# Kernel tuning notes

Hardware: AMD Instinct MI355X
Metric: run time of the kernel (lower is better)

Reference implementation:

```python
import jax, jax.numpy as jnp
import numpy as np

N, T, IN_DIM = 5000, 100, 32
FEAT, HID, OUT, HEADS = 64, 64, 8, 4
E = 160000
F_IN = FEAT + OUT  # GATCell input = concat(embedding, theta)


def setup_inputs() -> dict:
    key = jax.random.key(0)
    ks = jax.random.split(key, 16)
    s = 0.05
    d = {}
    d["x"] = jax.random.normal(ks[0], (N, T, IN_DIM), jnp.float32)
    d["edge_index"] = jax.random.randint(ks[1], (2, E), 0, N, dtype=jnp.int32)
    # LSTM params (PyTorch gate order: i, f, g, o)
    d["W_ih"] = jax.random.normal(ks[2], (IN_DIM, 4 * FEAT), jnp.float32) * s
    d["W_hh"] = jax.random.normal(ks[3], (FEAT, 4 * FEAT), jnp.float32) * s
    d["b_ih"] = jax.random.normal(ks[4], (4 * FEAT,), jnp.float32) * s
    d["b_hh"] = jax.random.normal(ks[5], (4 * FEAT,), jnp.float32) * s
    # TransformerConv params (lin_q/k/v with bias, lin_skip with bias; concat=False)
    d["Wq"] = jax.random.normal(ks[6], (F_IN, HEADS * HID), jnp.float32) * s
    d["bq"] = jax.random.normal(ks[7], (HEADS * HID,), jnp.float32) * s
    d["Wk"] = jax.random.normal(ks[8], (F_IN, HEADS * HID), jnp.float32) * s
    d["bk"] = jax.random.normal(ks[9], (HEADS * HID,), jnp.float32) * s
    d["Wv"] = jax.random.normal(ks[10], (F_IN, HEADS * HID), jnp.float32) * s
    d["bv"] = jax.random.normal(ks[11], (HEADS * HID,), jnp.float32) * s
    d["Wskip"] = jax.random.normal(ks[12], (F_IN, HID), jnp.float32) * s
    d["bskip"] = jax.random.normal(ks[13], (HID,), jnp.float32) * s
    # GATCell mlp (bias=False)
    d["Wmlp"] = jax.random.normal(ks[14], (HID, OUT), jnp.float32) * s
    return d


def _lstm(x, W_ih, W_hh, b_ih, b_hh):
    # x: [N, T, IN_DIM] -> embedding [T, N, FEAT]
    xs = jnp.transpose(x, (1, 0, 2))

    def step(carry, xt):
        h, c = carry
        gates = xt @ W_ih + h @ W_hh + (b_ih + b_hh)
        i, f, g, o = jnp.split(gates, 4, axis=-1)
        c = jax.nn.sigmoid(f) * c + jax.nn.sigmoid(i) * jnp.tanh(g)
        h = jax.nn.sigmoid(o) * jnp.tanh(c)
        return (h, c), h

    h0 = jnp.zeros((x.shape[0], FEAT), x.dtype)
    _, hs = jax.lax.scan(step, (h0, h0), xs)
    return hs


def _transformer_conv(h, edge_index, Wq, bq, Wk, bk, Wv, bv, Wskip, bskip):
    # h: [N, F_IN]; edge_index: [2, E] (row 0 = source j, row 1 = target i)
    n = h.shape[0]
    src, dst = edge_index[0], edge_index[1]
    q = (h @ Wq + bq).reshape(n, HEADS, HID)
    k = (h @ Wk + bk).reshape(n, HEADS, HID)
    v = (h @ Wv + bv).reshape(n, HEADS, HID)
    # per-edge attention logits [E, HEADS]
    alpha = jnp.einsum('ehd,ehd->eh', q[dst], k[src]) / jnp.sqrt(jnp.float32(HID))
    # segment softmax over incoming edges of each target node
    m = jax.ops.segment_max(alpha, dst, num_segments=n)
    m = jnp.where(jnp.isfinite(m), m, 0.0)
    ex = jnp.exp(alpha - m[dst])
    denom = jax.ops.segment_sum(ex, dst, num_segments=n)
    w = ex / jnp.maximum(denom[dst], 1e-16)
    agg = jax.ops.segment_sum(w[:, :, None] * v[src], dst, num_segments=n)  # [N,H,D]
    out = agg.mean(axis=1)  # concat=False -> average heads
    return out + h @ Wskip + bskip  # root skip connection


def reference(x, edge_index, W_ih, W_hh, b_ih, b_hh, Wq, bq, Wk, bk, Wv, bv,
              Wskip, bskip, Wmlp):
    emb = _lstm(x, W_ih, W_hh, b_ih, b_hh)  # [T, N, FEAT]
    n = x.shape[0]

    def gat_step(theta, emb_t):
        h_in = jnp.concatenate([emb_t, theta], axis=-1)  # [N, F_IN]
        hid = _transformer_conv(h_in, edge_index, Wq, bq, Wk, bk, Wv, bv,
                                Wskip, bskip)
        theta_new = jnp.tanh(hid) @ Wmlp
        return theta_new, theta_new

    theta0 = jnp.zeros((n, OUT), x.dtype)
    _, thetas = jax.lax.scan(gat_step, theta0, emb)  # [T, N, OUT]
    theta = jnp.transpose(thetas, (1, 0, 2))  # [N, T, OUT]

    alpha_beta = theta[:, :, :-3]
    a_b = jax.nn.sigmoid(theta[:, :, -3:-1])
    a = a_b[:, :, 0:1] * a_b[:, :, 1:]
    b = a_b[:, :, 0:1] - a
    c = jax.nn.softplus(theta[:, :, -1:])
    return jnp.concatenate([alpha_beta, a, b, c], axis=-1)
```

## Files before the change

### kernel.cpp

```cpp
#include <hip/hip_runtime.h>
#include <math.h>

#define NN 5000
#define TT 100
#define IND 32
#define FEATD 64
#define HIDD 64
#define OUTD 8
#define NHEADS 4
#define EE 160000
#define FIN 72
#define NHC 256

typedef unsigned short ushortx4 __attribute__((ext_vector_type(4)));
typedef float floatx2 __attribute__((ext_vector_type(2)));

__device__ __forceinline__ float fsig(float x){ return 1.f/(1.f+__expf(-x)); }
__device__ __forceinline__ float ftanh(float x){ return 1.f - 2.f/(__expf(2.f*x)+1.f); }
__device__ __forceinline__ float fsoftplus(float x){ return (x>20.f)? x : log1pf(__expf(x)); }

__global__ __launch_bounds__(256) void count_edges(const int* __restrict__ dst,
                                                   int* __restrict__ cnt){
    int e = blockIdx.x*256 + threadIdx.x;
    if (e < EE) atomicAdd(&cnt[dst[e]], 1);
}

#define SCAN_N 5120
__global__ __launch_bounds__(1024) void scan_csr(const int* __restrict__ cnt,
                                                 int* __restrict__ row_ptr,
                                                 int* __restrict__ cursor){
    __shared__ int sa[SCAN_N];
    __shared__ int sb[SCAN_N];
    int tid = threadIdx.x;
    for (int i=tid;i<SCAN_N;i+=1024) sa[i] = (i<NN)?cnt[i]:0;
    __syncthreads();
    int *s=sa, *d=sb;
    for (int off=1; off<SCAN_N; off<<=1){
        for (int i=tid;i<SCAN_N;i+=1024){
            int v = s[i];
            if (i>=off) v += s[i-off];
            d[i] = v;
        }
        __syncthreads();
        int* t=s; s=d; d=t;
    }
    for (int i=tid;i<=NN;i+=1024){
        int excl = (i==0)?0:s[i-1];
        row_ptr[i] = excl;
        if (i<NN) cursor[i] = excl;
    }
}

__global__ __launch_bounds__(256) void fill_edges(const int* __restrict__ src,
                                                  const int* __restrict__ dst,
                                                  int* __restrict__ cursor,
                                                  int* __restrict__ col){
    int e = blockIdx.x*256 + threadIdx.x;
    if (e < EE){
        int dn = dst[e];
        int pos = atomicAdd(&cursor[dn], 1);
        col[pos] = src[e];
    }
}

__global__ __launch_bounds__(256) void lstm_qkv_step(
    const float* __restrict__ x,
    const float* __restrict__ W_ih, const float* __restrict__ W_hh,
    const float* __restrict__ b_ih, const float* __restrict__ b_hh,
    const float* __restrict__ Wq, const float* __restrict__ bq,
    const float* __restrict__ Wk, const float* __restrict__ bk,
    const float* __restrict__ Wv, const float* __restrict__ bv,
    const float* __restrict__ Wsk, const float* __restrict__ bsk,
    float* __restrict__ h, float* __restrict__ c,
    const float* __restrict__ theta,
    float* __restrict__ q, float* __restrict__ sk,
    unsigned char* __restrict__ kv, int t)
{
    __shared__ float xh[8][96];
    __shared__ float hin[8][72];
    int n0 = blockIdx.x * 8;
    int tid = threadIdx.x;
    for (int i=tid; i<8*96; i+=256){
        int node = i/96, kk = i%96;
        int n = n0 + node;
        xh[node][kk] = (kk<32) ? x[(n*TT + t)*IND + kk] : h[n*64 + (kk-32)];
    }
    if (tid < 64){
        int node = tid>>3, j = tid&7;
        hin[node][64+j] = theta[(n0+node)*8 + j];
    }
    __syncthreads();

    int d  = tid & 63;
    int wv = tid >> 6;
    float acc[2][4];
    #pragma unroll
    for (int p=0;p<2;p++){
        #pragma unroll
        for (int g=0;g<4;g++) acc[p][g]=0.f;
    }
    #pragma unroll 8
    for (int kk=0; kk<32; kk++){
        const float* Wr = W_ih + kk*256;
        float w0=Wr[d], w1=Wr[d+64], w2=Wr[d+128], w3=Wr[d+192];
        float x0 = xh[wv][kk], x1 = xh[wv+4][kk];
        acc[0][0]=fmaf(x0,w0,acc[0][0]); acc[0][1]=fmaf(x0,w1,acc[0][1]);
        acc[0][2]=fmaf(x0,w2,acc[0][2]); acc[0][3]=fmaf(x0,w3,acc[0][3]);
        acc[1][0]=fmaf(x1,w0,acc[1][0]); acc[1][1]=fmaf(x1,w1,acc[1][1]);
        acc[1][2]=fmaf(x1,w2,acc[1][2]); acc[1][3]=fmaf(x1,w3,acc[1][3]);
    }
    #pragma unroll 8
    for (int kk=0; kk<64; kk++){
        const float* Wr = W_hh + kk*256;
        float w0=Wr[d], w1=Wr[d+64], w2=Wr[d+128], w3=Wr[d+192];
        float x0 = xh[wv][32+kk], x1 = xh[wv+4][32+kk];
        acc[0][0]=fmaf(x0,w0,acc[0][0]); acc[0][1]=fmaf(x0,w1,acc[0][1]);
        acc[0][2]=fmaf(x0,w2,acc[0][2]); acc[0][3]=fmaf(x0,w3,acc[0][3]);
        acc[1][0]=fmaf(x1,w0,acc[1][0]); acc[1][1]=fmaf(x1,w1,acc[1][1]);
        acc[1][2]=fmaf(x1,w2,acc[1][2]); acc[1][3]=fmaf(x1,w3,acc[1][3]);
    }
    float bi0 = b_ih[d]     + b_hh[d];
    float bi1 = b_ih[d+64]  + b_hh[d+64];
    float bi2 = b_ih[d+128] + b_hh[d+128];
    float bi3 = b_ih[d+192] + b_hh[d+192];
    #pragma unroll
    for (int p=0;p<2;p++){
        int node = wv + p*4;
        int n = n0 + node;
        float gi = fsig (acc[p][0] + bi0);
        float gf = fsig (acc[p][1] + bi1);
        float gg = ftanh(acc[p][2] + bi2);
        float go = fsig (acc[p][3] + bi3);
        float cold = c[n*64 + d];
        float cnew = gf*cold + gi*gg;
        float hnew = go*ftanh(cnew);
        c[n*64 + d] = cnew;
        h[n*64 + d] = hnew;
        hin[node][d] = hnew;
    }
    __syncthreads();

    if (tid < 208){
        int c4 = tid*4;
        const float* W; const float* b; int ncol; int cc; int kind;
        if (c4 < 256)      { W=Wq;  b=bq;  ncol=256; cc=c4;     kind=0; }
        else if (c4 < 512) { W=Wk;  b=bk;  ncol=256; cc=c4-256; kind=1; }
        else if (c4 < 768) { W=Wv;  b=bv;  ncol=256; cc=c4-512; kind=2; }
        else               { W=Wsk; b=bsk; ncol=64;  cc=c4-768; kind=3; }
        float acc2[8][4];
        #pragma unroll
        for (int nn=0;nn<8;nn++){
            #pragma unroll
            for (int j=0;j<4;j++) acc2[nn][j]=0.f;
        }
        #pragma unroll 4
        for (int kk=0; kk<FIN; kk++){
            float4 w = *reinterpret_cast<const float4*>(W + kk*ncol + cc);
            #pragma unroll
            for (int nn=0;nn<8;nn++){
                float xv = hin[nn][kk];
                acc2[nn][0]=fmaf(xv,w.x,acc2[nn][0]);
                acc2[nn][1]=fmaf(xv,w.y,acc2[nn][1]);
                acc2[nn][2]=fmaf(xv,w.z,acc2[nn][2]);
                acc2[nn][3]=fmaf(xv,w.w,acc2[nn][3]);
            }
        }
        float4 bb = *reinterpret_cast<const float4*>(b + cc);
        #pragma unroll
        for (int nn=0;nn<8;nn++){
            int n = n0 + nn;
            float o0=acc2[nn][0]+bb.x, o1=acc2[nn][1]+bb.y;
            float o2=acc2[nn][2]+bb.z, o3=acc2[nn][3]+bb.w;
            if (kind == 0){
                float4 o = {o0,o1,o2,o3};
                *reinterpret_cast<float4*>(q + n*NHC + cc) = o;
            } else if (kind == 3){
                float4 o = {o0,o1,o2,o3};
                *reinterpret_cast<float4*>(sk + n*64 + cc) = o;
            } else {
                int pk = __builtin_amdgcn_cvt_pk_fp8_f32(o0, o1, 0,  false);
                pk     = __builtin_amdgcn_cvt_pk_fp8_f32(o2, o3, pk, true);
                int off = n*512 + cc*2 + ((kind==2)?4:0);
                *reinterpret_cast<unsigned int*>(kv + off) = (unsigned int)pk;
            }
        }
    }
}

#define LOADKV(e) (*reinterpret_cast<const uint2*>(kv + (size_t)col[(e)]*512 + lane*8))
__global__ __launch_bounds__(256) void attn_step(const float* __restrict__ q,
                                                 const unsigned char* __restrict__ kv,
                                                 const float* __restrict__ sk,
                                                 const int* __restrict__ row_ptr,
                                                 const int* __restrict__ col,
                                                 const float* __restrict__ Wmlp,
                                                 float* __restrict__ theta,
                                                 float* __restrict__ out,
                                                 int t){
    __shared__ float mrg[2][5][64];
    int wvid = threadIdx.x >> 6;
    int lane = threadIdx.x & 63;
    int ln   = wvid >> 1;
    int half = wvid & 1;
    int n = blockIdx.x*2 + ln;
    int e0 = row_ptr[n], e1 = row_ptr[n+1];
    float4 qv = *reinterpret_cast<const float4*>(q + n*NHC + lane*4);
    qv.x *= 0.125f; qv.y *= 0.125f; qv.z *= 0.125f; qv.w *= 0.125f;

    float denA=0.f, denB=0.f;
    float aA0=0.f, aA1=0.f, aA2=0.f, aA3=0.f;
    float aB0=0.f, aB1=0.f, aB2=0.f, aB3=0.f;

    const uint2 zv = {0u,0u};
    uint2 bA0=zv, bA1=zv, bB0=zv, bB1=zv;
    int base = e0 + half;
    if (base     < e1) bA0 = LOADKV(base);
    if (base + 2 < e1) bB0 = LOADKV(base+2);
    if (base + 4 < e1) bA1 = LOADKV(base+4);
    if (base + 6 < e1) bB1 = LOADKV(base+6);
    for (int e = base; e < e1; e += 4){
        uint2 uA = bA0; bA0 = bA1; bA1 = zv;
        uint2 uB = bB0; bB0 = bB1; bB1 = zv;
        if (e + 8  < e1) bA1 = LOADKV(e+8);
        if (e + 10 < e1) bB1 = LOADKV(e+10);

        floatx2 kA0 = __builtin_amdgcn_cvt_pk_f32_fp8(uA.x, false);
        floatx2 kA1 = __builtin_amdgcn_cvt_pk_f32_fp8(uA.x, true);
        floatx2 kB0 = __builtin_amdgcn_cvt_pk_f32_fp8(uB.x, false);
        floatx2 kB1 = __builtin_amdgcn_cvt_pk_f32_fp8(uB.x, true);
        float pA = qv.x*kA0[0] + qv.y*kA0[1] + qv.z*kA1[0] + qv.w*kA1[1];
        float pB = qv.x*kB0[0] + qv.y*kB0[1] + qv.z*kB1[0] + qv.w*kB1[1];
        pA += __shfl_xor(pA,1); pB += __shfl_xor(pB,1);
        pA += __shfl_xor(pA,2); pB += __shfl_xor(pB,2);
        pA += __shfl_xor(pA,4); pB += __shfl_xor(pB,4);
        pA += __shfl_xor(pA,8); pB += __shfl_xor(pB,8);

        float eA = __expf(pA);
        float eB = __expf((e + 2 < e1) ? pB : -INFINITY);
        floatx2 vA0 = __builtin_amdgcn_cvt_pk_f32_fp8(uA.y, false);
        floatx2 vA1 = __builtin_amdgcn_cvt_pk_f32_fp8(uA.y, true);
        floatx2 vB0 = __builtin_amdgcn_cvt_pk_f32_fp8(uB.y, false);
        floatx2 vB1 = __builtin_amdgcn_cvt_pk_f32_fp8(uB.y, true);
        denA += eA;
        aA0 = fmaf(eA, vA0[0], aA0);
        aA1 = fmaf(eA, vA0[1], aA1);
        aA2 = fmaf(eA, vA1[0], aA2);
        aA3 = fmaf(eA, vA1[1], aA3);
        denB += eB;
        aB0 = fmaf(eB, vB0[0], aB0);
        aB1 = fmaf(eB, vB0[1], aB1);
        aB2 = fmaf(eB, vB1[0], aB2);
        aB3 = fmaf(eB, vB1[1], aB3);
    }
    float denom = denA + denB;
    float ax = aA0 + aB0;
    float ay = aA1 + aB1;
    float az = aA2 + aB2;
    float aw = aA3 + aB3;

    if (half == 1){
        mrg[ln][0][lane]=denom;
        mrg[ln][1][lane]=ax; mrg[ln][2][lane]=ay;
        mrg[ln][3][lane]=az; mrg[ln][4][lane]=aw;
    }
    __syncthreads();
    if (half == 1) return;

    denom += mrg[ln][0][lane];
    ax += mrg[ln][1][lane];
    ay += mrg[ln][2][lane];
    az += mrg[ln][3][lane];
    aw += mrg[ln][4][lane];

    float inv = 1.f / fmaxf(denom, 1e-16f);
    ax *= inv; ay *= inv; az *= inv; aw *= inv;
    ax += __shfl_xor(ax,16); ax += __shfl_xor(ax,32);
    ay += __shfl_xor(ay,16); ay += __shfl_xor(ay,32);
    az += __shfl_xor(az,16); az += __shfl_xor(az,32);
    aw += __shfl_xor(aw,16); aw += __shfl_xor(aw,32);
    int d0 = (lane & 15) * 4;
    float4 skv = *reinterpret_cast<const float4*>(sk + n*64 + d0);
    float t0 = ftanh(0.25f*ax + skv.x);
    float t1 = ftanh(0.25f*ay + skv.y);
    float t2 = ftanh(0.25f*az + skv.z);
    float t3 = ftanh(0.25f*aw + skv.w);
    float p8[8];
    #pragma unroll
    for (int j=0;j<8;j++){
        p8[j] = fmaf(t0, Wmlp[(d0+0)*8+j],
                fmaf(t1, Wmlp[(d0+1)*8+j],
                fmaf(t2, Wmlp[(d0+2)*8+j],
                     t3* Wmlp[(d0+3)*8+j])));
    }
    #pragma unroll
    for (int j=0;j<8;j++){
        p8[j] += __shfl_xor(p8[j],1);
        p8[j] += __shfl_xor(p8[j],2);
        p8[j] += __shfl_xor(p8[j],4);
        p8[j] += __shfl_xor(p8[j],8);
    }
    if (lane == 0){
        float4 t0v = {p8[0],p8[1],p8[2],p8[3]};
        float4 t1v = {p8[4],p8[5],p8[6],p8[7]};
        *reinterpret_cast<float4*>(theta + n*8)     = t0v;
        *reinterpret_cast<float4*>(theta + n*8 + 4) = t1v;
        float ab0 = fsig(p8[5]);
        float ab1 = fsig(p8[6]);
        float a  = ab0*ab1;
        float bb = ab0 - a;
        float cc = fsoftplus(p8[7]);
        float4 o0 = {p8[0],p8[1],p8[2],p8[3]};
        float4 o1 = {p8[4],a,bb,cc};
        float* op = out + ((size_t)n*TT + t)*8;
        *reinterpret_cast<float4*>(op)     = o0;
        *reinterpret_cast<float4*>(op + 4) = o1;
    }
}

extern "C" void kernel_launch(void* const* d_in, const int* in_sizes, int n_in,
                              void* d_out, int out_size, void* d_ws, size_t ws_size,
                              hipStream_t stream) {
    const float* x     = (const float*)d_in[0];
    const int*   ei    = (const int*)  d_in[1];
    const float* W_ih  = (const float*)d_in[2];
    const float* W_hh  = (const float*)d_in[3];
    const float* b_ih  = (const float*)d_in[4];
    const float* b_hh  = (const float*)d_in[5];
    const float* Wq    = (const float*)d_in[6];
    const float* bq    = (const float*)d_in[7];
    const float* Wk    = (const float*)d_in[8];
    const float* bk    = (const float*)d_in[9];
    const float* Wv    = (const float*)d_in[10];
    const float* bv    = (const float*)d_in[11];
    const float* Wsk   = (const float*)d_in[12];
    const float* bsk   = (const float*)d_in[13];
    const float* Wmlp  = (const float*)d_in[14];
    float* out = (float*)d_out;

    float* f = (float*)d_ws;
    float* h     = f;
    float* c     = h + NN*64;
    float* theta = c + NN*64;
    float* q     = theta + NN*8;
    float* skb   = q + NN*NHC;
    unsigned char* kvb = (unsigned char*)(skb + NN*64);
    int* ip      = (int*)(kvb + (size_t)NN*512);
    int* row_ptr = ip;
    int* cnt     = row_ptr + (NN+1);
    int* cursor  = cnt + NN;
    int* colv    = cursor + NN;

    const int* src = ei;
    const int* dst = ei + EE;

    hipMemsetAsync(h, 0, (size_t)NN*(64+64+8)*sizeof(float), stream);
    hipMemsetAsync(cnt, 0, (size_t)NN*sizeof(int), stream);

    count_edges<<<(EE+255)/256, 256, 0, stream>>>(dst, cnt);
    scan_csr<<<1, 1024, 0, stream>>>(cnt, row_ptr, cursor);
    fill_edges<<<(EE+255)/256, 256, 0, stream>>>(src, dst, cursor, colv);

    for (int t=0; t<TT; t++){
        lstm_qkv_step<<<NN/8, 256, 0, stream>>>(x, W_ih, W_hh, b_ih, b_hh,
                                                Wq,bq, Wk,bk, Wv,bv, Wsk,bsk,
                                                h, c, theta, q, skb, kvb, t);
        attn_step<<<NN/2, 256, 0, stream>>>(q, kvb, skb, row_ptr, colv, Wmlp,
                                            theta, out, t);
    }
}
```

Baseline: 5.113 ms.

## Overlap LSTM step t with attention step t-1 in one fused launch

```diff
diff --git a/kernel.cpp b/kernel.cpp
--- a/kernel.cpp
+++ b/kernel.cpp
@@ -11,8 +11,9 @@
 #define EE 160000
 #define FIN 72
 #define NHC 256
-
-typedef unsigned short ushortx4 __attribute__((ext_vector_type(4)));
+#define ATTN_B 2500
+#define LSTM_B 625
+
 typedef float floatx2 __attribute__((ext_vector_type(2)));
 
 __device__ __forceinline__ float fsig(float x){ return 1.f/(1.f+__expf(-x)); }
@@ -63,80 +64,219 @@
     }
 }
 
-__global__ __launch_bounds__(256) void lstm_qkv_step(
+#define LOADKV(e) (*reinterpret_cast<const uint2*>(kv + (size_t)col[(e)]*512 + lane*8))
+__global__ __launch_bounds__(256) void lstm_attn_step(
     const float* __restrict__ x,
     const float* __restrict__ W_ih, const float* __restrict__ W_hh,
     const float* __restrict__ b_ih, const float* __restrict__ b_hh,
+    float* __restrict__ h, float* __restrict__ c,
+    const float* __restrict__ q,
+    const unsigned char* __restrict__ kv,
+    const float* __restrict__ sk,
+    const int* __restrict__ row_ptr,
+    const int* __restrict__ col,
+    const float* __restrict__ Wmlp,
+    float* __restrict__ theta,
+    float* __restrict__ out,
+    int t)
+{
+    __shared__ float mrg[2][5][64];
+    __shared__ float xh[8][96];
+    int tid = threadIdx.x;
+
+    if (blockIdx.x < ATTN_B){
+        if (t == 0) return;
+        int wvid = tid >> 6;
+        int lane = tid & 63;
+        int ln   = wvid >> 1;
+        int half = wvid & 1;
+        int n = blockIdx.x*2 + ln;
+        int e0 = row_ptr[n], e1 = row_ptr[n+1];
+        float4 qv = *reinterpret_cast<const float4*>(q + n*NHC + lane*4);
+        qv.x *= 0.125f; qv.y *= 0.125f; qv.z *= 0.125f; qv.w *= 0.125f;
+
+        float denA=0.f, denB=0.f;
+        float aA0=0.f, aA1=0.f, aA2=0.f, aA3=0.f;
+        float aB0=0.f, aB1=0.f, aB2=0.f, aB3=0.f;
+
+        const uint2 zv = {0u,0u};
+        uint2 bA0=zv, bA1=zv, bB0=zv, bB1=zv;
+        int base = e0 + half;
+        if (base     < e1) bA0 = LOADKV(base);
+        if (base + 2 < e1) bB0 = LOADKV(base+2);
+        if (base + 4 < e1) bA1 = LOADKV(base+4);
+        if (base + 6 < e1) bB1 = LOADKV(base+6);
+        for (int e = base; e < e1; e += 4){
+            uint2 uA = bA0; bA0 = bA1; bA1 = zv;
+            uint2 uB = bB0; bB0 = bB1; bB1 = zv;
+            if (e + 8  < e1) bA1 = LOADKV(e+8);
+            if (e + 10 < e1) bB1 = LOADKV(e+10);
+
+            floatx2 kA0 = __builtin_amdgcn_cvt_pk_f32_fp8(uA.x, false);
+            floatx2 kA1 = __builtin_amdgcn_cvt_pk_f32_fp8(uA.x, true);
+            floatx2 kB0 = __builtin_amdgcn_cvt_pk_f32_fp8(uB.x, false);
+            floatx2 kB1 = __builtin_amdgcn_cvt_pk_f32_fp8(uB.x, true);
+            float pA = qv.x*kA0[0] + qv.y*kA0[1] + qv.z*kA1[0] + qv.w*kA1[1];
+            float pB = qv.x*kB0[0] + qv.y*kB0[1] + qv.z*kB1[0] + qv.w*kB1[1];
+            pA += __shfl_xor(pA,1); pB += __shfl_xor(pB,1);
+            pA += __shfl_xor(pA,2); pB += __shfl_xor(pB,2);
+            pA += __shfl_xor(pA,4); pB += __shfl_xor(pB,4);
+            pA += __shfl_xor(pA,8); pB += __shfl_xor(pB,8);
+
+            float eA = __expf(pA);
+            float eB = __expf((e + 2 < e1) ? pB : -INFINITY);
+            floatx2 vA0 = __builtin_amdgcn_cvt_pk_f32_fp8(uA.y, false);
+            floatx2 vA1 = __builtin_amdgcn_cvt_pk_f32_fp8(uA.y, true);
+            floatx2 vB0 = __builtin_amdgcn_cvt_pk_f32_fp8(uB.y, false);
+            floatx2 vB1 = __builtin_amdgcn_cvt_pk_f32_fp8(uB.y, true);
+            denA += eA;
+            aA0 = fmaf(eA, vA0[0], aA0);
+            aA1 = fmaf(eA, vA0[1], aA1);
+            aA2 = fmaf(eA, vA1[0], aA2);
+            aA3 = fmaf(eA, vA1[1], aA3);
+            denB += eB;
+            aB0 = fmaf(eB, vB0[0], aB0);
+            aB1 = fmaf(eB, vB0[1], aB1);
+            aB2 = fmaf(eB, vB1[0], aB2);
+            aB3 = fmaf(eB, vB1[1], aB3);
+        }
+        float denom = denA + denB;
+        float ax = aA0 + aB0;
+        float ay = aA1 + aB1;
+        float az = aA2 + aB2;
+        float aw = aA3 + aB3;
+
+        if (half == 1){
+            mrg[ln][0][lane]=denom;
+            mrg[ln][1][lane]=ax; mrg[ln][2][lane]=ay;
+            mrg[ln][3][lane]=az; mrg[ln][4][lane]=aw;
+        }
+        __syncthreads();
+        if (half == 1) return;
+
+        denom += mrg[ln][0][lane];
+        ax += mrg[ln][1][lane];
+        ay += mrg[ln][2][lane];
+        az += mrg[ln][3][lane];
+        aw += mrg[ln][4][lane];
+
+        float inv = 1.f / fmaxf(denom, 1e-16f);
+        ax *= inv; ay *= inv; az *= inv; aw *= inv;
+        ax += __shfl_xor(ax,16); ax += __shfl_xor(ax,32);
+        ay += __shfl_xor(ay,16); ay += __shfl_xor(ay,32);
+        az += __shfl_xor(az,16); az += __shfl_xor(az,32);
+        aw += __shfl_xor(aw,16); aw += __shfl_xor(aw,32);
+        int d0 = (lane & 15) * 4;
+        float4 skv = *reinterpret_cast<const float4*>(sk + n*64 + d0);
+        float t0 = ftanh(0.25f*ax + skv.x);
+        float t1 = ftanh(0.25f*ay + skv.y);
+        float t2 = ftanh(0.25f*az + skv.z);
+        float t3 = ftanh(0.25f*aw + skv.w);
+        float p8[8];
+        #pragma unroll
+        for (int j=0;j<8;j++){
+            p8[j] = fmaf(t0, Wmlp[(d0+0)*8+j],
+                    fmaf(t1, Wmlp[(d0+1)*8+j],
+                    fmaf(t2, Wmlp[(d0+2)*8+j],
+                         t3* Wmlp[(d0+3)*8+j])));
+        }
+        #pragma unroll
+        for (int j=0;j<8;j++){
+            p8[j] += __shfl_xor(p8[j],1);
+            p8[j] += __shfl_xor(p8[j],2);
+            p8[j] += __shfl_xor(p8[j],4);
+            p8[j] += __shfl_xor(p8[j],8);
+        }
+        if (lane == 0){
+            float4 t0v = {p8[0],p8[1],p8[2],p8[3]};
+            float4 t1v = {p8[4],p8[5],p8[6],p8[7]};
+            *reinterpret_cast<float4*>(theta + n*8)     = t0v;
+            *reinterpret_cast<float4*>(theta + n*8 + 4) = t1v;
+            float ab0 = fsig(p8[5]);
+            float ab1 = fsig(p8[6]);
+            float a  = ab0*ab1;
+            float bb = ab0 - a;
+            float cc = fsoftplus(p8[7]);
+            float4 o0 = {p8[0],p8[1],p8[2],p8[3]};
+            float4 o1 = {p8[4],a,bb,cc};
+            float* op = out + ((size_t)n*TT + (t-1))*8;
+            *reinterpret_cast<float4*>(op)     = o0;
+            *reinterpret_cast<float4*>(op + 4) = o1;
+        }
+    } else {
+        if (t >= TT) return;
+        int n0 = (blockIdx.x - ATTN_B) * 8;
+        for (int i=tid; i<8*96; i+=256){
+            int node = i/96, kk = i%96;
+            int n = n0 + node;
+            xh[node][kk] = (kk<32) ? x[(n*TT + t)*IND + kk] : h[n*64 + (kk-32)];
+        }
+        __syncthreads();
+
+        int d  = tid & 63;
+        int wv = tid >> 6;
+        float acc[2][4];
+        #pragma unroll
+        for (int p=0;p<2;p++){
+            #pragma unroll
+            for (int g=0;g<4;g++) acc[p][g]=0.f;
+        }
+        #pragma unroll 8
+        for (int kk=0; kk<32; kk++){
+            const float* Wr = W_ih + kk*256;
+            float w0=Wr[d], w1=Wr[d+64], w2=Wr[d+128], w3=Wr[d+192];
+            float x0 = xh[wv][kk], x1 = xh[wv+4][kk];
+            acc[0][0]=fmaf(x0,w0,acc[0][0]); acc[0][1]=fmaf(x0,w1,acc[0][1]);
+            acc[0][2]=fmaf(x0,w2,acc[0][2]); acc[0][3]=fmaf(x0,w3,acc[0][3]);
+            acc[1][0]=fmaf(x1,w0,acc[1][0]); acc[1][1]=fmaf(x1,w1,acc[1][1]);
+            acc[1][2]=fmaf(x1,w2,acc[1][2]); acc[1][3]=fmaf(x1,w3,acc[1][3]);
+        }
+        #pragma unroll 8
+        for (int kk=0; kk<64; kk++){
+            const float* Wr = W_hh + kk*256;
+            float w0=Wr[d], w1=Wr[d+64], w2=Wr[d+128], w3=Wr[d+192];
+            float x0 = xh[wv][32+kk], x1 = xh[wv+4][32+kk];
+            acc[0][0]=fmaf(x0,w0,acc[0][0]); acc[0][1]=fmaf(x0,w1,acc[0][1]);
+            acc[0][2]=fmaf(x0,w2,acc[0][2]); acc[0][3]=fmaf(x0,w3,acc[0][3]);
+            acc[1][0]=fmaf(x1,w0,acc[1][0]); acc[1][1]=fmaf(x1,w1,acc[1][1]);
+            acc[1][2]=fmaf(x1,w2,acc[1][2]); acc[1][3]=fmaf(x1,w3,acc[1][3]);
+        }
+        float bi0 = b_ih[d]     + b_hh[d];
+        float bi1 = b_ih[d+64]  + b_hh[d+64];
+        float bi2 = b_ih[d+128] + b_hh[d+128];
+        float bi3 = b_ih[d+192] + b_hh[d+192];
+        #pragma unroll
+        for (int p=0;p<2;p++){
+            int n = n0 + wv + p*4;
+            float gi = fsig (acc[p][0] + bi0);
+            float gf = fsig (acc[p][1] + bi1);
+            float gg = ftanh(acc[p][2] + bi2);
+            float go = fsig (acc[p][3] + bi3);
+            float cold = c[n*64 + d];
+            float cnew = gf*cold + gi*gg;
+            float hnew = go*ftanh(cnew);
+            c[n*64 + d] = cnew;
+            h[n*64 + d] = hnew;
+        }
+    }
+}
+
+__global__ __launch_bounds__(256) void qkv_step(
+    const float* __restrict__ h, const float* __restrict__ theta,
     const float* __restrict__ Wq, const float* __restrict__ bq,
     const float* __restrict__ Wk, const float* __restrict__ bk,
     const float* __restrict__ Wv, const float* __restrict__ bv,
     const float* __restrict__ Wsk, const float* __restrict__ bsk,
-    float* __restrict__ h, float* __restrict__ c,
-    const float* __restrict__ theta,
     float* __restrict__ q, float* __restrict__ sk,
-    unsigned char* __restrict__ kv, int t)
+    unsigned char* __restrict__ kv)
 {
-    __shared__ float xh[8][96];
     __shared__ float hin[8][72];
     int n0 = blockIdx.x * 8;
     int tid = threadIdx.x;
-    for (int i=tid; i<8*96; i+=256){
-        int node = i/96, kk = i%96;
+    for (int i=tid; i<8*72; i+=256){
+        int node = i/72, kk = i%72;
         int n = n0 + node;
-        xh[node][kk] = (kk<32) ? x[(n*TT + t)*IND + kk] : h[n*64 + (kk-32)];
-    }
-    if (tid < 64){
-        int node = tid>>3, j = tid&7;
-        hin[node][64+j] = theta[(n0+node)*8 + j];
-    }
-    __syncthreads();
-
-    int d  = tid & 63;
-    int wv = tid >> 6;
-    float acc[2][4];
-    #pragma unroll
-    for (int p=0;p<2;p++){
-        #pragma unroll
-        for (int g=0;g<4;g++) acc[p][g]=0.f;
-    }
-    #pragma unroll 8
-    for (int kk=0; kk<32; kk++){
-        const float* Wr = W_ih + kk*256;
-        float w0=Wr[d], w1=Wr[d+64], w2=Wr[d+128], w3=Wr[d+192];
-        float x0 = xh[wv][kk], x1 = xh[wv+4][kk];
-        acc[0][0]=fmaf(x0,w0,acc[0][0]); acc[0][1]=fmaf(x0,w1,acc[0][1]);
-        acc[0][2]=fmaf(x0,w2,acc[0][2]); acc[0][3]=fmaf(x0,w3,acc[0][3]);
-        acc[1][0]=fmaf(x1,w0,acc[1][0]); acc[1][1]=fmaf(x1,w1,acc[1][1]);
-        acc[1][2]=fmaf(x1,w2,acc[1][2]); acc[1][3]=fmaf(x1,w3,acc[1][3]);
-    }
-    #pragma unroll 8
-    for (int kk=0; kk<64; kk++){
-        const float* Wr = W_hh + kk*256;
-        float w0=Wr[d], w1=Wr[d+64], w2=Wr[d+128], w3=Wr[d+192];
-        float x0 = xh[wv][32+kk], x1 = xh[wv+4][32+kk];
-        acc[0][0]=fmaf(x0,w0,acc[0][0]); acc[0][1]=fmaf(x0,w1,acc[0][1]);
-        acc[0][2]=fmaf(x0,w2,acc[0][2]); acc[0][3]=fmaf(x0,w3,acc[0][3]);
-        acc[1][0]=fmaf(x1,w0,acc[1][0]); acc[1][1]=fmaf(x1,w1,acc[1][1]);
-        acc[1][2]=fmaf(x1,w2,acc[1][2]); acc[1][3]=fmaf(x1,w3,acc[1][3]);
-    }
-    float bi0 = b_ih[d]     + b_hh[d];
-    float bi1 = b_ih[d+64]  + b_hh[d+64];
-    float bi2 = b_ih[d+128] + b_hh[d+128];
-    float bi3 = b_ih[d+192] + b_hh[d+192];
-    #pragma unroll
-    for (int p=0;p<2;p++){
-        int node = wv + p*4;
-        int n = n0 + node;
-        float gi = fsig (acc[p][0] + bi0);
-        float gf = fsig (acc[p][1] + bi1);
-        float gg = ftanh(acc[p][2] + bi2);
-        float go = fsig (acc[p][3] + bi3);
-        float cold = c[n*64 + d];
-        float cnew = gf*cold + gi*gg;
-        float hnew = go*ftanh(cnew);
-        c[n*64 + d] = cnew;
-        h[n*64 + d] = hnew;
-        hin[node][d] = hnew;
+        hin[node][kk] = (kk<64) ? h[n*64+kk] : theta[n*8 + (kk-64)];
     }
     __syncthreads();
 
@@ -184,136 +324,6 @@
                 *reinterpret_cast<unsigned int*>(kv + off) = (unsigned int)pk;
             }
         }
-    }
-}
-
-#define LOADKV(e) (*reinterpret_cast<const uint2*>(kv + (size_t)col[(e)]*512 + lane*8))
-__global__ __launch_bounds__(256) void attn_step(const float* __restrict__ q,
-                                                 const unsigned char* __restrict__ kv,
-                                                 const float* __restrict__ sk,
-                                                 const int* __restrict__ row_ptr,
-                                                 const int* __restrict__ col,
-                                                 const float* __restrict__ Wmlp,
-                                                 float* __restrict__ theta,
-                                                 float* __restrict__ out,
-                                                 int t){
-    __shared__ float mrg[2][5][64];
-    int wvid = threadIdx.x >> 6;
-    int lane = threadIdx.x & 63;
-    int ln   = wvid >> 1;
-    int half = wvid & 1;
-    int n = blockIdx.x*2 + ln;
-    int e0 = row_ptr[n], e1 = row_ptr[n+1];
-    float4 qv = *reinterpret_cast<const float4*>(q + n*NHC + lane*4);
-    qv.x *= 0.125f; qv.y *= 0.125f; qv.z *= 0.125f; qv.w *= 0.125f;
-
-    float denA=0.f, denB=0.f;
-    float aA0=0.f, aA1=0.f, aA2=0.f, aA3=0.f;
-    float aB0=0.f, aB1=0.f, aB2=0.f, aB3=0.f;
-
-    const uint2 zv = {0u,0u};
-    uint2 bA0=zv, bA1=zv, bB0=zv, bB1=zv;
-    int base = e0 + half;
-    if (base     < e1) bA0 = LOADKV(base);
-    if (base + 2 < e1) bB0 = LOADKV(base+2);
-    if (base + 4 < e1) bA1 = LOADKV(base+4);
-    if (base + 6 < e1) bB1 = LOADKV(base+6);
-    for (int e = base; e < e1; e += 4){
-        uint2 uA = bA0; bA0 = bA1; bA1 = zv;
-        uint2 uB = bB0; bB0 = bB1; bB1 = zv;
-        if (e + 8  < e1) bA1 = LOADKV(e+8);
-        if (e + 10 < e1) bB1 = LOADKV(e+10);
-
-        floatx2 kA0 = __builtin_amdgcn_cvt_pk_f32_fp8(uA.x, false);
-        floatx2 kA1 = __builtin_amdgcn_cvt_pk_f32_fp8(uA.x, true);
-        floatx2 kB0 = __builtin_amdgcn_cvt_pk_f32_fp8(uB.x, false);
-        floatx2 kB1 = __builtin_amdgcn_cvt_pk_f32_fp8(uB.x, true);
-        float pA = qv.x*kA0[0] + qv.y*kA0[1] + qv.z*kA1[0] + qv.w*kA1[1];
-        float pB = qv.x*kB0[0] + qv.y*kB0[1] + qv.z*kB1[0] + qv.w*kB1[1];
-        pA += __shfl_xor(pA,1); pB += __shfl_xor(pB,1);
-        pA += __shfl_xor(pA,2); pB += __shfl_xor(pB,2);
-        pA += __shfl_xor(pA,4); pB += __shfl_xor(pB,4);
-        pA += __shfl_xor(pA,8); pB += __shfl_xor(pB,8);
-
-        float eA = __expf(pA);
-        float eB = __expf((e + 2 < e1) ? pB : -INFINITY);
-        floatx2 vA0 = __builtin_amdgcn_cvt_pk_f32_fp8(uA.y, false);
-        floatx2 vA1 = __builtin_amdgcn_cvt_pk_f32_fp8(uA.y, true);
-        floatx2 vB0 = __builtin_amdgcn_cvt_pk_f32_fp8(uB.y, false);
-        floatx2 vB1 = __builtin_amdgcn_cvt_pk_f32_fp8(uB.y, true);
-        denA += eA;
-        aA0 = fmaf(eA, vA0[0], aA0);
-        aA1 = fmaf(eA, vA0[1], aA1);
-        aA2 = fmaf(eA, vA1[0], aA2);
-        aA3 = fmaf(eA, vA1[1], aA3);
-        denB += eB;
-        aB0 = fmaf(eB, vB0[0], aB0);
-        aB1 = fmaf(eB, vB0[1], aB1);
-        aB2 = fmaf(eB, vB1[0], aB2);
-        aB3 = fmaf(eB, vB1[1], aB3);
-    }
-    float denom = denA + denB;
-    float ax = aA0 + aB0;
-    float ay = aA1 + aB1;
-    float az = aA2 + aB2;
-    float aw = aA3 + aB3;
-
-    if (half == 1){
-        mrg[ln][0][lane]=denom;
-        mrg[ln][1][lane]=ax; mrg[ln][2][lane]=ay;
-        mrg[ln][3][lane]=az; mrg[ln][4][lane]=aw;
-    }
-    __syncthreads();
-    if (half == 1) return;
-
-    denom += mrg[ln][0][lane];
-    ax += mrg[ln][1][lane];
-    ay += mrg[ln][2][lane];
-    az += mrg[ln][3][lane];
-    aw += mrg[ln][4][lane];
-
-    float inv = 1.f / fmaxf(denom, 1e-16f);
-    ax *= inv; ay *= inv; az *= inv; aw *= inv;
-    ax += __shfl_xor(ax,16); ax += __shfl_xor(ax,32);
-    ay += __shfl_xor(ay,16); ay += __shfl_xor(ay,32);
-    az += __shfl_xor(az,16); az += __shfl_xor(az,32);
-    aw += __shfl_xor(aw,16); aw += __shfl_xor(aw,32);
-    int d0 = (lane & 15) * 4;
-    float4 skv = *reinterpret_cast<const float4*>(sk + n*64 + d0);
-    float t0 = ftanh(0.25f*ax + skv.x);
-    float t1 = ftanh(0.25f*ay + skv.y);
-    float t2 = ftanh(0.25f*az + skv.z);
-    float t3 = ftanh(0.25f*aw + skv.w);
-    float p8[8];
-    #pragma unroll
-    for (int j=0;j<8;j++){
-        p8[j] = fmaf(t0, Wmlp[(d0+0)*8+j],
-                fmaf(t1, Wmlp[(d0+1)*8+j],
-                fmaf(t2, Wmlp[(d0+2)*8+j],
-                     t3* Wmlp[(d0+3)*8+j])));
-    }
-    #pragma unroll
-    for (int j=0;j<8;j++){
-        p8[j] += __shfl_xor(p8[j],1);
-        p8[j] += __shfl_xor(p8[j],2);
-        p8[j] += __shfl_xor(p8[j],4);
-        p8[j] += __shfl_xor(p8[j],8);
-    }
-    if (lane == 0){
-        float4 t0v = {p8[0],p8[1],p8[2],p8[3]};
-        float4 t1v = {p8[4],p8[5],p8[6],p8[7]};
-        *reinterpret_cast<float4*>(theta + n*8)     = t0v;
-        *reinterpret_cast<float4*>(theta + n*8 + 4) = t1v;
-        float ab0 = fsig(p8[5]);
-        float ab1 = fsig(p8[6]);
-        float a  = ab0*ab1;
-        float bb = ab0 - a;
-        float cc = fsoftplus(p8[7]);
-        float4 o0 = {p8[0],p8[1],p8[2],p8[3]};
-        float4 o1 = {p8[4],a,bb,cc};
-        float* op = out + ((size_t)n*TT + t)*8;
-        *reinterpret_cast<float4*>(op)     = o0;
-        *reinterpret_cast<float4*>(op + 4) = o1;
     }
 }
 
@@ -360,11 +370,12 @@
     scan_csr<<<1, 1024, 0, stream>>>(cnt, row_ptr, cursor);
     fill_edges<<<(EE+255)/256, 256, 0, stream>>>(src, dst, cursor, colv);
 
-    for (int t=0; t<TT; t++){
-        lstm_qkv_step<<<NN/8, 256, 0, stream>>>(x, W_ih, W_hh, b_ih, b_hh,
-                                                Wq,bq, Wk,bk, Wv,bv, Wsk,bsk,
-                                                h, c, theta, q, skb, kvb, t);
-        attn_step<<<NN/2, 256, 0, stream>>>(q, kvb, skb, row_ptr, colv, Wmlp,
-                                            theta, out, t);
-    }
-}
+    for (int t=0; t<=TT; t++){
+        lstm_attn_step<<<ATTN_B + LSTM_B, 256, 0, stream>>>(
+            x, W_ih, W_hh, b_ih, b_hh, h, c,
+            q, kvb, skb, row_ptr, colv, Wmlp, theta, out, t);
+        if (t < TT)
+            qkv_step<<<LSTM_B, 256, 0, stream>>>(h, theta,
+                Wq,bq, Wk,bk, Wv,bv, Wsk,bsk, q, skb, kvb);
+    }
+}
```

Measured after the change: 4.762 ms. -6.9%, faster.
